# Kernel tuning notes

Measured on AMD Instinct MI355X. Metric: run time of the kernel, lower is better.

## Reference

```python
import jax, jax.numpy as jnp
import numpy as np

N_NODES = 50000
N_EDGES = 400000
N_GRAPHS = 500
N_FEAT = 4
EMB = 200
HID = 128


def setup_inputs() -> dict:
    key = jax.random.key(0)
    ks = jax.random.split(key, 16)
    x = jax.random.normal(ks[0], (N_NODES, N_FEAT), dtype=jnp.float32)
    edge_index = jax.random.randint(ks[1], (2, N_EDGES), 0, N_NODES, dtype=jnp.int64)
    x_scalar = jax.random.normal(ks[2], (N_GRAPHS, N_FEAT), dtype=jnp.float32)
    batch_index = jnp.sort(jax.random.randint(ks[3], (N_NODES,), 0, N_GRAPHS, dtype=jnp.int64))

    def lin(k, fan_in, fan_out):
        return jax.random.normal(k, (fan_in, fan_out), dtype=jnp.float32) / np.sqrt(fan_in)

    params = {
        'W0': lin(ks[4], N_FEAT, EMB), 'b0': jnp.zeros((EMB,), jnp.float32),
        'W1': lin(ks[5], EMB, EMB), 'b1': jnp.zeros((EMB,), jnp.float32),
        'W2': lin(ks[6], EMB, EMB), 'b2': jnp.zeros((EMB,), jnp.float32),
        'W3': lin(ks[7], EMB, EMB), 'b3': jnp.zeros((EMB,), jnp.float32),
        'Wl1': lin(ks[8], EMB + N_FEAT, HID),
        'bl1': jax.random.normal(ks[9], (HID,), jnp.float32) * 0.01,
        'Wl2': lin(ks[10], HID, 1),
        'bl2': jax.random.normal(ks[11], (1,), jnp.float32) * 0.01,
    }
    return dict(x=x, edge_index=edge_index, x_scalar=x_scalar, batch_index=batch_index, **params)


def _gcn_conv(h, W, b, src, dst, norm, num_nodes):
    # PyG GCNConv: h' = D^-1/2 (A+I) D^-1/2 (h W) + b, with precomputed edge norms
    m = (h @ W)[src] * norm[:, None]            # [E+N, out]
    out = jax.ops.segment_sum(m, dst, num_segments=num_nodes)
    return out + b


def reference(x, edge_index, x_scalar, batch_index,
              W0, b0, W1, b1, W2, b2, W3, b3, Wl1, bl1, Wl2, bl2):
    num_nodes = x.shape[0]
    loops = jnp.arange(num_nodes, dtype=edge_index.dtype)
    src = jnp.concatenate([edge_index[0], loops])  # self-loops appended
    dst = jnp.concatenate([edge_index[1], loops])
    deg = jax.ops.segment_sum(jnp.ones_like(dst, dtype=x.dtype), dst, num_segments=num_nodes)
    dinv = deg ** -0.5                              # deg >= 1 due to self-loops
    norm = dinv[src] * dinv[dst]

    h = jax.nn.leaky_relu(_gcn_conv(x, W0, b0, src, dst, norm, num_nodes), 0.01)
    h = jax.nn.leaky_relu(_gcn_conv(h, W1, b1, src, dst, norm, num_nodes), 0.01)
    h = jax.nn.leaky_relu(_gcn_conv(h, W2, b2, src, dst, norm, num_nodes), 0.01)
    h = jax.nn.leaky_relu(_gcn_conv(h, W3, b3, src, dst, norm, num_nodes), 0.01)

    # global mean pool per graph
    sums = jax.ops.segment_sum(h, batch_index, num_segments=N_GRAPHS)
    cnt = jax.ops.segment_sum(jnp.ones((num_nodes,), h.dtype), batch_index, num_segments=N_GRAPHS)
    pooled = sums / jnp.maximum(cnt, 1.0)[:, None]

    g = jnp.concatenate([pooled, x_scalar], axis=1)   # [G, EMB+4]
    g = jax.nn.leaky_relu(g @ Wl1 + bl1, 0.01)
    out = g @ Wl2 + bl2                                # [G, 1]
    return out
```

## Files before the change

### kernel.cpp

```cpp
#include <hip/hip_runtime.h>
#include <math.h>

#define LEAKY(v) ((v) > 0.0f ? (v) : 0.01f * (v))

typedef _Float16 v8h __attribute__((ext_vector_type(8)));
typedef float v4f __attribute__((ext_vector_type(4)));

__global__ void k_count(const int* __restrict__ ei, int* __restrict__ cnt, int E) {
    int e = blockIdx.x * blockDim.x + threadIdx.x;
    if (e < E) atomicAdd(&cnt[ei[E + e]], 1);
}

__global__ __launch_bounds__(256) void k_scan1(const int* __restrict__ cnt,
                                               int* __restrict__ rowptr,
                                               int* __restrict__ bsum, int n) {
    __shared__ int s[256];
    int t = threadIdx.x, i = blockIdx.x * 256 + t;
    int v = (i < n) ? cnt[i] : 0;
    s[t] = v;
    __syncthreads();
    for (int off = 1; off < 256; off <<= 1) {
        int u = (t >= off) ? s[t - off] : 0;
        __syncthreads();
        s[t] += u;
        __syncthreads();
    }
    if (i < n) rowptr[i] = s[t] - v;
    if (t == 255) bsum[blockIdx.x] = s[255];
}

__global__ __launch_bounds__(256) void k_scan3(int* __restrict__ rowptr,
                                               const int* __restrict__ bsum,
                                               const int* __restrict__ cnt,
                                               float* __restrict__ dinv, int n,
                                               float* __restrict__ pooled, int npool) {
    __shared__ int sred[256];
    int t = threadIdx.x;
    int accum = 0;
    for (int b = t; b < (int)blockIdx.x; b += 256) accum += bsum[b];
    sred[t] = accum;
    __syncthreads();
    for (int off = 128; off > 0; off >>= 1) {
        if (t < off) sred[t] += sred[t + off];
        __syncthreads();
    }
    int base = sred[0];
    int i = blockIdx.x * 256 + t;
    if (i < n) {
        rowptr[i] += base;
        dinv[i] = rsqrtf(1.0f + (float)cnt[i]);
    }
    for (int j = i; j < npool; j += gridDim.x * 256) pooled[j] = 0.0f;
}

__global__ void k_fill(const int* __restrict__ ei, const float* __restrict__ dinv,
                       int* __restrict__ rowptr, int2* __restrict__ adj, int E) {
    int e = blockIdx.x * blockDim.x + threadIdx.x;
    if (e < E) {
        int s = ei[e], d = ei[E + e];
        int pos = atomicAdd(&rowptr[d], 1);
        adj[pos] = make_int2(s, __float_as_int(dinv[s] * dinv[d]));
    }
}

__global__ __launch_bounds__(256) void k_splitW3(const float* __restrict__ W1,
                                                 const float* __restrict__ W2,
                                                 const float* __restrict__ W3,
                                                 _Float16* __restrict__ th0, _Float16* __restrict__ tl0,
                                                 _Float16* __restrict__ th1, _Float16* __restrict__ tl1,
                                                 _Float16* __restrict__ th2, _Float16* __restrict__ tl2,
                                                 int* __restrict__ cnt, int n) {
    int layer = blockIdx.y;
    const float* W = (layer == 0) ? W1 : (layer == 1) ? W2 : W3;
    _Float16* Wth = (layer == 0) ? th0 : (layer == 1) ? th1 : th2;
    _Float16* Wtl = (layer == 0) ? tl0 : (layer == 1) ? tl1 : tl2;
    int idx = blockIdx.x * blockDim.x + threadIdx.x;
    int gidx = (blockIdx.y * gridDim.x + blockIdx.x) * 256 + threadIdx.x;
    for (int j = gidx; j < n; j += gridDim.x * gridDim.y * 256) cnt[j] = 0;
    if (idx >= 224 * 208) return;
    int k = idx / 208, c = idx - k * 208;
    float v = (k < 200 && c < 200) ? W[k * 200 + c] : 0.0f;
    _Float16 hi = (_Float16)v;
    _Float16 lo = (_Float16)(v - (float)hi);
    Wth[c * 224 + k] = hi;
    Wtl[c * 224 + k] = lo;
}

__global__ __launch_bounds__(512, 4) void k_gemm200_mfma_l0(const float* __restrict__ x,
                                                            const float* __restrict__ dinv,
                                                            const int* __restrict__ rowptr,
                                                            const int2* __restrict__ adj,
                                                            const float* __restrict__ W0,
                                                            const float* __restrict__ b0,
                                                            const _Float16* __restrict__ Wth,
                                                            const _Float16* __restrict__ Wtl,
                                                            _Float16* __restrict__ T, int M) {
    __shared__ _Float16 Wsh[2][208 * 32];
    __shared__ _Float16 Wsl[2][208 * 32];
    __shared__ float W0s[4][200];
    __shared__ float b0s[200];
    const int tid  = threadIdx.x;
    const int lane = tid & 63;
    const int wid  = tid >> 6;
    const int quad = lane >> 4;
    const int l16  = lane & 15;
    const int rowA = blockIdx.x * 128 + wid * 16 + l16;
    const int rowAc = min(rowA, M - 1);

    const int nr0 = tid >> 2, p0 = tid & 3;
    const bool two = (tid < 320);
    const int nr1 = nr0 + 128;
    uint4 rh0, rl0, rh1, rl1;
    rh0 = *(const uint4*)&Wth[nr0 * 224 + p0 * 8];
    rl0 = *(const uint4*)&Wtl[nr0 * 224 + p0 * 8];
    if (two) {
        rh1 = *(const uint4*)&Wth[nr1 * 224 + p0 * 8];
        rl1 = *(const uint4*)&Wtl[nr1 * 224 + p0 * 8];
    }

    for (int idx = tid; idx < 1000; idx += 512) {
        if (idx < 800) W0s[idx / 200][idx % 200] = W0[idx];
        else b0s[idx - 800] = b0[idx - 800];
    }

    float w0n = dinv[rowAc]; w0n *= w0n;
    float4 xv = ((const float4*)x)[rowAc];
    float4 pxv = make_float4(xv.x * w0n, xv.y * w0n, xv.z * w0n, xv.w * w0n);
    {
        int lo = rowAc ? rowptr[rowAc - 1] : 0;
        int hi = rowptr[rowAc];
        for (int j = lo; j < hi; ++j) {
            int2 cw = adj[j];
            float w = __int_as_float(cw.y);
            float4 sv = ((const float4*)x)[cw.x];
            pxv.x += sv.x * w; pxv.y += sv.y * w; pxv.z += sv.z * w; pxv.w += sv.w * w;
        }
    }

    v4f acc[13];
#pragma unroll
    for (int t = 0; t < 13; ++t) acc[t] = 0.0f;

#pragma unroll
    for (int kc = 0; kc < 7; ++kc) {
        const int k0 = kc * 32;
        const int buf = kc & 1;
        *(uint4*)&Wsh[buf][nr0 * 32 + p0 * 8] = rh0;
        *(uint4*)&Wsl[buf][nr0 * 32 + p0 * 8] = rl0;
        if (two) {
            *(uint4*)&Wsh[buf][nr1 * 32 + p0 * 8] = rh1;
            *(uint4*)&Wsl[buf][nr1 * 32 + p0 * 8] = rl1;
        }
        if (kc < 6) {
            rh0 = *(const uint4*)&Wth[nr0 * 224 + (k0 + 32) + p0 * 8];
            rl0 = *(const uint4*)&Wtl[nr0 * 224 + (k0 + 32) + p0 * 8];
            if (two) {
                rh1 = *(const uint4*)&Wth[nr1 * 224 + (k0 + 32) + p0 * 8];
                rl1 = *(const uint4*)&Wtl[nr1 * 224 + (k0 + 32) + p0 * 8];
            }
        }
        __syncthreads();
        v8h ah, al;
        int kb = k0 + quad * 8;
        if (kb < 200) {
#pragma unroll
            for (int j = 0; j < 8; ++j) {
                int k = kb + j;
                float pv = pxv.x * W0s[0][k] + pxv.y * W0s[1][k]
                         + pxv.z * W0s[2][k] + pxv.w * W0s[3][k] + b0s[k];
                pv = LEAKY(pv);
                _Float16 h = (_Float16)pv;
                ah[j] = h;
                al[j] = (_Float16)(pv - (float)h);
            }
        } else {
#pragma unroll
            for (int j = 0; j < 8; ++j) { ah[j] = (_Float16)0.0f; al[j] = (_Float16)0.0f; }
        }
#pragma unroll
        for (int t = 0; t < 13; ++t) {
            int nidx = (t * 16 + l16) * 32 + quad * 8;
            v8h wh = *(const v8h*)&Wsh[buf][nidx];
            v8h wl = *(const v8h*)&Wsl[buf][nidx];
            acc[t] = __builtin_amdgcn_mfma_f32_16x16x32_f16(ah, wh, acc[t], 0, 0, 0);
            acc[t] = __builtin_amdgcn_mfma_f32_16x16x32_f16(ah, wl, acc[t], 0, 0, 0);
            acc[t] = __builtin_amdgcn_mfma_f32_16x16x32_f16(al, wh, acc[t], 0, 0, 0);
        }
    }
    const int rb = blockIdx.x * 128 + wid * 16 + quad * 4;
#pragma unroll
    for (int t = 0; t < 13; ++t) {
        int c = t * 16 + l16;
        if (c < 200) {
#pragma unroll
            for (int e = 0; e < 4; ++e) {
                int r = rb + e;
                if (r < M) T[(size_t)r * 200 + c] = (_Float16)acc[t][e];
            }
        }
    }
}

__global__ __launch_bounds__(512, 4) void k_gemm200_mfma(const _Float16* __restrict__ P,
                                                         const float* __restrict__ bias,
                                                         const _Float16* __restrict__ Wth,
                                                         const _Float16* __restrict__ Wtl,
                                                         _Float16* __restrict__ T, int M) {
    __shared__ _Float16 Wsh[2][208 * 32];
    __shared__ _Float16 Wsl[2][208 * 32];
    __shared__ float bS[200];
    const int tid  = threadIdx.x;
    const int lane = tid & 63;
    const int wid  = tid >> 6;
    const int quad = lane >> 4;
    const int l16  = lane & 15;
    const int rowA = blockIdx.x * 128 + wid * 16 + l16;
    const int rowAc = min(rowA, M - 1);
    const _Float16* Prow = P + (size_t)rowAc * 200;

    const int nr0 = tid >> 2, p0 = tid & 3;
    const bool two = (tid < 320);
    const int nr1 = nr0 + 128;
    uint4 rh0, rl0, rh1, rl1;
    rh0 = *(const uint4*)&Wth[nr0 * 224 + p0 * 8];
    rl0 = *(const uint4*)&Wtl[nr0 * 224 + p0 * 8];
    if (two) {
        rh1 = *(const uint4*)&Wth[nr1 * 224 + p0 * 8];
        rl1 = *(const uint4*)&Wtl[nr1 * 224 + p0 * 8];
    }
    if (tid < 200) bS[tid] = bias[tid];

    v8h pch[7];
#pragma unroll
    for (int kc = 0; kc < 7; ++kc) {
        int kb = kc * 32 + quad * 8;
        if (kb < 200) {
            pch[kc] = *(const v8h*)(Prow + kb);
        } else {
#pragma unroll
            for (int j = 0; j < 8; ++j) pch[kc][j] = (_Float16)0.0f;
        }
    }

    v4f acc[13];
#pragma unroll
    for (int t = 0; t < 13; ++t) acc[t] = 0.0f;

#pragma unroll
    for (int kc = 0; kc < 7; ++kc) {
        const int k0 = kc * 32;
        const int buf = kc & 1;
        *(uint4*)&Wsh[buf][nr0 * 32 + p0 * 8] = rh0;
        *(uint4*)&Wsl[buf][nr0 * 32 + p0 * 8] = rl0;
        if (two) {
            *(uint4*)&Wsh[buf][nr1 * 32 + p0 * 8] = rh1;
            *(uint4*)&Wsl[buf][nr1 * 32 + p0 * 8] = rl1;
        }
        if (kc < 6) {
            rh0 = *(const uint4*)&Wth[nr0 * 224 + (k0 + 32) + p0 * 8];
            rl0 = *(const uint4*)&Wtl[nr0 * 224 + (k0 + 32) + p0 * 8];
            if (two) {
                rh1 = *(const uint4*)&Wth[nr1 * 224 + (k0 + 32) + p0 * 8];
                rl1 = *(const uint4*)&Wtl[nr1 * 224 + (k0 + 32) + p0 * 8];
            }
        }
        __syncthreads();
        v8h ah, al;
        int kb = k0 + quad * 8;
        if (kb < 200) {
            v8h ph = pch[kc];
#pragma unroll
            for (int j = 0; j < 8; ++j) {
                float av = (float)ph[j] + bS[kb + j];
                av = LEAKY(av);
                _Float16 h = (_Float16)av;
                ah[j] = h;
                al[j] = (_Float16)(av - (float)h);
            }
        } else {
#pragma unroll
            for (int j = 0; j < 8; ++j) { ah[j] = (_Float16)0.0f; al[j] = (_Float16)0.0f; }
        }
#pragma unroll
        for (int t = 0; t < 13; ++t) {
            int nidx = (t * 16 + l16) * 32 + quad * 8;
            v8h wh = *(const v8h*)&Wsh[buf][nidx];
            v8h wl = *(const v8h*)&Wsl[buf][nidx];
            acc[t] = __builtin_amdgcn_mfma_f32_16x16x32_f16(ah, wh, acc[t], 0, 0, 0);
            acc[t] = __builtin_amdgcn_mfma_f32_16x16x32_f16(ah, wl, acc[t], 0, 0, 0);
            acc[t] = __builtin_amdgcn_mfma_f32_16x16x32_f16(al, wh, acc[t], 0, 0, 0);
        }
    }
    const int rb = blockIdx.x * 128 + wid * 16 + quad * 4;
#pragma unroll
    for (int t = 0; t < 13; ++t) {
        int c = t * 16 + l16;
        if (c < 200) {
#pragma unroll
            for (int e = 0; e < 4; ++e) {
                int r = rb + e;
                if (r < M) T[(size_t)r * 200 + c] = (_Float16)acc[t][e];
            }
        }
    }
}

__global__ __launch_bounds__(256) void k_gather200h(const _Float16* __restrict__ t,
                                                    const float* __restrict__ dinv,
                                                    const int* __restrict__ rowptr,
                                                    const int2* __restrict__ adj,
                                                    _Float16* __restrict__ p, int n) {
    int gid = blockIdx.x * blockDim.x + threadIdx.x;
    if (gid >= n * 25) return;
    int v = gid / 25, c8 = gid - v * 25;
    const v8h* tp = (const v8h*)t;
    float w0 = dinv[v]; w0 *= w0;
    v8h tv = tp[v * 25 + c8];
    float a0[8], a1[8], a2[8], a3[8];
#pragma unroll
    for (int i = 0; i < 8; ++i) { a0[i] = (float)tv[i] * w0; a1[i] = 0.0f; a2[i] = 0.0f; a3[i] = 0.0f; }
    int lo = v ? rowptr[v - 1] : 0;
    int hi = rowptr[v];
    int j = lo;
    for (; j + 3 < hi; j += 4) {
        int2 e0 = adj[j], e1 = adj[j + 1], e2 = adj[j + 2], e3 = adj[j + 3];
        float wa = __int_as_float(e0.y), wb = __int_as_float(e1.y);
        float wc = __int_as_float(e2.y), wd = __int_as_float(e3.y);
        v8h s0 = tp[e0.x * 25 + c8];
        v8h s1 = tp[e1.x * 25 + c8];
        v8h s2 = tp[e2.x * 25 + c8];
        v8h s3 = tp[e3.x * 25 + c8];
#pragma unroll
        for (int i = 0; i < 8; ++i) {
            a0[i] += (float)s0[i] * wa;
            a1[i] += (float)s1[i] * wb;
            a2[i] += (float)s2[i] * wc;
            a3[i] += (float)s3[i] * wd;
        }
    }
    for (; j < hi; ++j) {
        int2 cw = adj[j];
        float w = __int_as_float(cw.y);
        v8h sv = tp[cw.x * 25 + c8];
#pragma unroll
        for (int i = 0; i < 8; ++i) a0[i] += (float)sv[i] * w;
    }
    v8h o;
#pragma unroll
    for (int i = 0; i < 8; ++i) o[i] = (_Float16)((a0[i] + a1[i]) + (a2[i] + a3[i]));
    ((v8h*)p)[v * 25 + c8] = o;
}

__global__ __launch_bounds__(256) void k_gpool(const _Float16* __restrict__ T,
                                               const float* __restrict__ dinv,
                                               const int* __restrict__ rowptr,
                                               const int2* __restrict__ adj,
                                               const float* __restrict__ b3,
                                               const int* __restrict__ batch, int n,
                                               float* __restrict__ pooled) {
    __shared__ float part[10][25][9];
    const int t = threadIdx.x;
    const int c8 = t % 25, li = t / 25;
    const int base = blockIdx.x * 32;
    const int end = min(base + 32, n);
    const v8h* tp = (const v8h*)T;
    float4 ba = *(const float4*)(b3 + c8 * 8);
    float4 bb = *(const float4*)(b3 + c8 * 8 + 4);
    float bv[8] = {ba.x, ba.y, ba.z, ba.w, bb.x, bb.y, bb.z, bb.w};

    int seg = base;
    while (seg < end) {
        int g = batch[seg];
        int lo2 = seg + 1, hi2 = end;
        while (lo2 < hi2) { int m = (lo2 + hi2) >> 1; if (batch[m] == g) lo2 = m + 1; else hi2 = m; }
        int segend = lo2;

        if (li < 10) {
            float acc[8];
#pragma unroll
            for (int i = 0; i < 8; ++i) acc[i] = 0.0f;
            for (int i = seg + li; i < segend; i += 10) {
                float w0 = dinv[i]; w0 *= w0;
                v8h tv = tp[(size_t)i * 25 + c8];
                float a0[8], a1[8];
#pragma unroll
                for (int q = 0; q < 8; ++q) { a0[q] = (float)tv[q] * w0; a1[q] = 0.0f; }
                int elo = i ? rowptr[i - 1] : 0;
                int ehi = rowptr[i];
                int j = elo;
                for (; j + 1 < ehi; j += 2) {
                    int2 e0 = adj[j], e1 = adj[j + 1];
                    float wa = __int_as_float(e0.y), wb = __int_as_float(e1.y);
                    v8h s0 = tp[(size_t)e0.x * 25 + c8];
                    v8h s1 = tp[(size_t)e1.x * 25 + c8];
#pragma unroll
                    for (int q = 0; q < 8; ++q) {
                        a0[q] += (float)s0[q] * wa;
                        a1[q] += (float)s1[q] * wb;
                    }
                }
                if (j < ehi) {
                    int2 cw = adj[j];
                    float w = __int_as_float(cw.y);
                    v8h sv = tp[(size_t)cw.x * 25 + c8];
#pragma unroll
                    for (int q = 0; q < 8; ++q) a0[q] += (float)sv[q] * w;
                }
#pragma unroll
                for (int q = 0; q < 8; ++q) {
                    float v = a0[q] + a1[q] + bv[q];
                    acc[q] += LEAKY(v);
                }
            }
#pragma unroll
            for (int q = 0; q < 8; ++q) part[li][c8][q] = acc[q];
        }
        __syncthreads();
        if (t < 200) {
            float s = 0.0f;
#pragma unroll
            for (int l2 = 0; l2 < 10; ++l2) s += part[l2][t >> 3][t & 7];
            atomicAdd(&pooled[g * 200 + t], s);
        }
        __syncthreads();
        seg = segend;
    }
}

__global__ __launch_bounds__(128) void k_headfin(const float* __restrict__ pooled,
                                                 const int* __restrict__ batch, int n_nodes,
                                                 const float* __restrict__ xs,
                                                 const float* __restrict__ Wl1,
                                                 const float* __restrict__ bl1,
                                                 const float* __restrict__ Wl2,
                                                 const float* __restrict__ bl2,
                                                 float* __restrict__ out) {
    __shared__ float grow[204];
    __shared__ float partial[2];
    __shared__ int sb[2];
    int g = blockIdx.x;
    int t = threadIdx.x;
    if (t == 0 || t == 64) {
        int target = g + (t ? 1 : 0);
        int lo = 0, hi = n_nodes;
        while (lo < hi) { int m = (lo + hi) >> 1; if (batch[m] < target) lo = m + 1; else hi = m; }
        sb[t ? 1 : 0] = lo;
    }
    __syncthreads();
    float inv = 1.0f / fmaxf((float)(sb[1] - sb[0]), 1.0f);
    for (int idx = t; idx < 200; idx += 128) grow[idx] = pooled[g * 200 + idx] * inv;
    if (t < 4) grow[200 + t] = xs[g * 4 + t];
    __syncthreads();
    float s = bl1[t];
    for (int k = 0; k < 204; ++k) s += grow[k] * Wl1[k * 128 + t];
    s = LEAKY(s);
    float hv = s * Wl2[t];
    for (int off = 32; off > 0; off >>= 1) hv += __shfl_down(hv, off, 64);
    if ((t & 63) == 0) partial[t >> 6] = hv;
    __syncthreads();
    if (t == 0) out[g] = partial[0] + partial[1] + bl2[0];
}

extern "C" void kernel_launch(void* const* d_in, const int* in_sizes, int n_in,
                              void* d_out, int out_size, void* d_ws, size_t ws_size,
                              hipStream_t stream) {
    const float* x    = (const float*)d_in[0];
    const int*   ei   = (const int*)d_in[1];
    const float* xs   = (const float*)d_in[2];
    const int*   batch= (const int*)d_in[3];
    const float* W0   = (const float*)d_in[4];
    const float* b0   = (const float*)d_in[5];
    const float* W1   = (const float*)d_in[6];
    const float* b1   = (const float*)d_in[7];
    const float* W2   = (const float*)d_in[8];
    const float* b2   = (const float*)d_in[9];
    const float* W3   = (const float*)d_in[10];
    const float* b3   = (const float*)d_in[11];
    const float* Wl1  = (const float*)d_in[12];
    const float* bl1  = (const float*)d_in[13];
    const float* Wl2  = (const float*)d_in[14];
    const float* bl2  = (const float*)d_in[15];
    float* out = (float*)d_out;

    const int N = in_sizes[0] / 4;
    const int E = in_sizes[1] / 2;
    const int G = in_sizes[2] / 4;

    char* ws = (char*)d_ws;
    size_t off = 0;
    auto alloc = [&](size_t bytes) { void* p = ws + off; off += (bytes + 255) & ~size_t(255); return p; };
    _Float16* bufA = (_Float16*)alloc((size_t)N * 200 * sizeof(_Float16));
    _Float16* bufB = (_Float16*)alloc((size_t)N * 200 * sizeof(_Float16));
    float* dinv   = (float*)alloc((size_t)N * sizeof(float));
    float* pooled = (float*)alloc((size_t)G * 200 * sizeof(float));
    int*   cnt    = (int*)alloc((size_t)N * sizeof(int));
    int*   rowptr = (int*)alloc(((size_t)N + 1) * sizeof(int));
    int*   bsum   = (int*)alloc(256 * sizeof(int));
    int2*  adj    = (int2*)alloc((size_t)E * sizeof(int2));
    _Float16* Wth[3]; _Float16* Wtl[3];
    for (int i = 0; i < 3; ++i) {
        Wth[i] = (_Float16*)alloc(208 * 224 * sizeof(_Float16));
        Wtl[i] = (_Float16*)alloc(208 * 224 * sizeof(_Float16));
    }

    const int B = 256;
    const int nblk = (N + 255) / 256;

    dim3 sg((224 * 208 + B - 1) / B, 3);
    k_splitW3<<<sg, B, 0, stream>>>(W1, W2, W3, Wth[0], Wtl[0], Wth[1], Wtl[1], Wth[2], Wtl[2],
                                    cnt, N);

    k_count<<<(E + B - 1) / B, B, 0, stream>>>(ei, cnt, E);
    k_scan1<<<nblk, 256, 0, stream>>>(cnt, rowptr, bsum, N);
    k_scan3<<<nblk, 256, 0, stream>>>(rowptr, bsum, cnt, dinv, N, pooled, G * 200);
    k_fill<<<(E + B - 1) / B, B, 0, stream>>>(ei, dinv, rowptr, adj, E);

    const int gblocks = (N * 25 + 255) / 256;
    const int mblocks = (N + 127) / 128;

    k_gemm200_mfma_l0<<<mblocks, 512, 0, stream>>>(x, dinv, rowptr, adj, W0, b0,
                                                   Wth[0], Wtl[0], bufA, N);
    k_gather200h<<<gblocks, 256, 0, stream>>>(bufA, dinv, rowptr, adj, bufB, N);

    k_gemm200_mfma<<<mblocks, 512, 0, stream>>>(bufB, b1, Wth[1], Wtl[1], bufA, N);
    k_gather200h<<<gblocks, 256, 0, stream>>>(bufA, dinv, rowptr, adj, bufB, N);
    k_gemm200_mfma<<<mblocks, 512, 0, stream>>>(bufB, b2, Wth[2], Wtl[2], bufA, N);

    k_gpool<<<(N + 31) / 32, 256, 0, stream>>>(bufA, dinv, rowptr, adj, b3, batch, N, pooled);
    k_headfin<<<G, 128, 0, stream>>>(pooled, batch, N, xs, Wl1, bl1, Wl2, bl2, out);
}
```

Baseline: 328.3 us.

## Fuse degree count into weight split, single-pass scan, unroll pooling gather by four

Moves zeroing of the count and pooled buffers to memsets and folds the edge degree counting into the weight-split kernel, removing one launch. The two-kernel block scan becomes one kernel in which every block re-reduces all preceding counts from global memory, which saves a launch but adds redundant reads that grow with the block index. In the pooling gather, the neighbor loop is unrolled to four independent accumulators to expose more memory-level parallelism, at some register cost.

New measurement: 359.9 us. 9.6% more time.

```diff
diff --git a/kernel.cpp b/kernel.cpp
--- a/kernel.cpp
+++ b/kernel.cpp
@@ -6,16 +6,48 @@
 typedef _Float16 v8h __attribute__((ext_vector_type(8)));
 typedef float v4f __attribute__((ext_vector_type(4)));
 
-__global__ void k_count(const int* __restrict__ ei, int* __restrict__ cnt, int E) {
-    int e = blockIdx.x * blockDim.x + threadIdx.x;
-    if (e < E) atomicAdd(&cnt[ei[E + e]], 1);
-}
-
-__global__ __launch_bounds__(256) void k_scan1(const int* __restrict__ cnt,
-                                               int* __restrict__ rowptr,
-                                               int* __restrict__ bsum, int n) {
+__global__ __launch_bounds__(256) void k_splitcount(const float* __restrict__ W1,
+                                                    const float* __restrict__ W2,
+                                                    const float* __restrict__ W3,
+                                                    _Float16* __restrict__ th0, _Float16* __restrict__ tl0,
+                                                    _Float16* __restrict__ th1, _Float16* __restrict__ tl1,
+                                                    _Float16* __restrict__ th2, _Float16* __restrict__ tl2,
+                                                    const int* __restrict__ ei, int* __restrict__ cnt,
+                                                    int E) {
+    int layer = blockIdx.y;
+    const float* W = (layer == 0) ? W1 : (layer == 1) ? W2 : W3;
+    _Float16* Wth = (layer == 0) ? th0 : (layer == 1) ? th1 : th2;
+    _Float16* Wtl = (layer == 0) ? tl0 : (layer == 1) ? tl1 : tl2;
+    int idx = blockIdx.x * blockDim.x + threadIdx.x;
+    int gidx = (blockIdx.y * gridDim.x + blockIdx.x) * 256 + threadIdx.x;
+    int gsz = gridDim.x * gridDim.y * 256;
+    for (int e = gidx; e < E; e += gsz) atomicAdd(&cnt[ei[E + e]], 1);
+    if (idx >= 224 * 208) return;
+    int k = idx / 208, c = idx - k * 208;
+    float v = (k < 200 && c < 200) ? W[k * 200 + c] : 0.0f;
+    _Float16 hi = (_Float16)v;
+    _Float16 lo = (_Float16)(v - (float)hi);
+    Wth[c * 224 + k] = hi;
+    Wtl[c * 224 + k] = lo;
+}
+
+__global__ __launch_bounds__(256) void k_scan(const int* __restrict__ cnt,
+                                              int* __restrict__ rowptr,
+                                              float* __restrict__ dinv, int n) {
     __shared__ int s[256];
-    int t = threadIdx.x, i = blockIdx.x * 256 + t;
+    __shared__ int sred[256];
+    int t = threadIdx.x;
+    int lim = blockIdx.x * 256;
+    int accum = 0;
+    for (int i = t; i < lim; i += 256) accum += cnt[i];
+    sred[t] = accum;
+    __syncthreads();
+    for (int off = 128; off > 0; off >>= 1) {
+        if (t < off) sred[t] += sred[t + off];
+        __syncthreads();
+    }
+    int base = sred[0];
+    int i = lim + t;
     int v = (i < n) ? cnt[i] : 0;
     s[t] = v;
     __syncthreads();
@@ -25,32 +57,10 @@
         s[t] += u;
         __syncthreads();
     }
-    if (i < n) rowptr[i] = s[t] - v;
-    if (t == 255) bsum[blockIdx.x] = s[255];
-}
-
-__global__ __launch_bounds__(256) void k_scan3(int* __restrict__ rowptr,
-                                               const int* __restrict__ bsum,
-                                               const int* __restrict__ cnt,
-                                               float* __restrict__ dinv, int n,
-                                               float* __restrict__ pooled, int npool) {
-    __shared__ int sred[256];
-    int t = threadIdx.x;
-    int accum = 0;
-    for (int b = t; b < (int)blockIdx.x; b += 256) accum += bsum[b];
-    sred[t] = accum;
-    __syncthreads();
-    for (int off = 128; off > 0; off >>= 1) {
-        if (t < off) sred[t] += sred[t + off];
-        __syncthreads();
-    }
-    int base = sred[0];
-    int i = blockIdx.x * 256 + t;
     if (i < n) {
-        rowptr[i] += base;
-        dinv[i] = rsqrtf(1.0f + (float)cnt[i]);
-    }
-    for (int j = i; j < npool; j += gridDim.x * 256) pooled[j] = 0.0f;
+        rowptr[i] = base + s[t] - v;
+        dinv[i] = rsqrtf(1.0f + (float)v);
+    }
 }
 
 __global__ void k_fill(const int* __restrict__ ei, const float* __restrict__ dinv,
@@ -61,29 +71,6 @@
         int pos = atomicAdd(&rowptr[d], 1);
         adj[pos] = make_int2(s, __float_as_int(dinv[s] * dinv[d]));
     }
-}
-
-__global__ __launch_bounds__(256) void k_splitW3(const float* __restrict__ W1,
-                                                 const float* __restrict__ W2,
-                                                 const float* __restrict__ W3,
-                                                 _Float16* __restrict__ th0, _Float16* __restrict__ tl0,
-                                                 _Float16* __restrict__ th1, _Float16* __restrict__ tl1,
-                                                 _Float16* __restrict__ th2, _Float16* __restrict__ tl2,
-                                                 int* __restrict__ cnt, int n) {
-    int layer = blockIdx.y;
-    const float* W = (layer == 0) ? W1 : (layer == 1) ? W2 : W3;
-    _Float16* Wth = (layer == 0) ? th0 : (layer == 1) ? th1 : th2;
-    _Float16* Wtl = (layer == 0) ? tl0 : (layer == 1) ? tl1 : tl2;
-    int idx = blockIdx.x * blockDim.x + threadIdx.x;
-    int gidx = (blockIdx.y * gridDim.x + blockIdx.x) * 256 + threadIdx.x;
-    for (int j = gidx; j < n; j += gridDim.x * gridDim.y * 256) cnt[j] = 0;
-    if (idx >= 224 * 208) return;
-    int k = idx / 208, c = idx - k * 208;
-    float v = (k < 200 && c < 200) ? W[k * 200 + c] : 0.0f;
-    _Float16 hi = (_Float16)v;
-    _Float16 lo = (_Float16)(v - (float)hi);
-    Wth[c * 224 + k] = hi;
-    Wtl[c * 224 + k] = lo;
 }
 
 __global__ __launch_bounds__(512, 4) void k_gemm200_mfma_l0(const float* __restrict__ x,
@@ -382,24 +369,31 @@
             for (int i = seg + li; i < segend; i += 10) {
                 float w0 = dinv[i]; w0 *= w0;
                 v8h tv = tp[(size_t)i * 25 + c8];
-                float a0[8], a1[8];
-#pragma unroll
-                for (int q = 0; q < 8; ++q) { a0[q] = (float)tv[q] * w0; a1[q] = 0.0f; }
+                float a0[8], a1[8], a2[8], a3[8];
+#pragma unroll
+                for (int q = 0; q < 8; ++q) {
+                    a0[q] = (float)tv[q] * w0; a1[q] = 0.0f; a2[q] = 0.0f; a3[q] = 0.0f;
+                }
                 int elo = i ? rowptr[i - 1] : 0;
                 int ehi = rowptr[i];
                 int j = elo;
-                for (; j + 1 < ehi; j += 2) {
-                    int2 e0 = adj[j], e1 = adj[j + 1];
+                for (; j + 3 < ehi; j += 4) {
+                    int2 e0 = adj[j], e1 = adj[j + 1], e2 = adj[j + 2], e3 = adj[j + 3];
                     float wa = __int_as_float(e0.y), wb = __int_as_float(e1.y);
+                    float wc = __int_as_float(e2.y), wd = __int_as_float(e3.y);
                     v8h s0 = tp[(size_t)e0.x * 25 + c8];
                     v8h s1 = tp[(size_t)e1.x * 25 + c8];
+                    v8h s2 = tp[(size_t)e2.x * 25 + c8];
+                    v8h s3 = tp[(size_t)e3.x * 25 + c8];
 #pragma unroll
                     for (int q = 0; q < 8; ++q) {
                         a0[q] += (float)s0[q] * wa;
                         a1[q] += (float)s1[q] * wb;
+                        a2[q] += (float)s2[q] * wc;
+                        a3[q] += (float)s3[q] * wd;
                     }
                 }
-                if (j < ehi) {
+                for (; j < ehi; ++j) {
                     int2 cw = adj[j];
                     float w = __int_as_float(cw.y);
                     v8h sv = tp[(size_t)cw.x * 25 + c8];
@@ -408,7 +402,7 @@
                 }
 #pragma unroll
                 for (int q = 0; q < 8; ++q) {
-                    float v = a0[q] + a1[q] + bv[q];
+                    float v = (a0[q] + a1[q]) + (a2[q] + a3[q]) + bv[q];
                     acc[q] += LEAKY(v);
                 }
             }
@@ -495,7 +489,6 @@
     float* pooled = (float*)alloc((size_t)G * 200 * sizeof(float));
     int*   cnt    = (int*)alloc((size_t)N * sizeof(int));
     int*   rowptr = (int*)alloc(((size_t)N + 1) * sizeof(int));
-    int*   bsum   = (int*)alloc(256 * sizeof(int));
     int2*  adj    = (int2*)alloc((size_t)E * sizeof(int2));
     _Float16* Wth[3]; _Float16* Wtl[3];
     for (int i = 0; i < 3; ++i) {
@@ -506,13 +499,14 @@
     const int B = 256;
     const int nblk = (N + 255) / 256;
 
+    hipMemsetAsync(cnt, 0, (size_t)N * sizeof(int), stream);
+    hipMemsetAsync(pooled, 0, (size_t)G * 200 * sizeof(float), stream);
+
     dim3 sg((224 * 208 + B - 1) / B, 3);
-    k_splitW3<<<sg, B, 0, stream>>>(W1, W2, W3, Wth[0], Wtl[0], Wth[1], Wtl[1], Wth[2], Wtl[2],
-                                    cnt, N);
-
-    k_count<<<(E + B - 1) / B, B, 0, stream>>>(ei, cnt, E);
-    k_scan1<<<nblk, 256, 0, stream>>>(cnt, rowptr, bsum, N);
-    k_scan3<<<nblk, 256, 0, stream>>>(rowptr, bsum, cnt, dinv, N, pooled, G * 200);
+    k_splitcount<<<sg, B, 0, stream>>>(W1, W2, W3, Wth[0], Wtl[0], Wth[1], Wtl[1], Wth[2], Wtl[2],
+                                       ei, cnt, E);
+
+    k_scan<<<nblk, 256, 0, stream>>>(cnt, rowptr, dinv, N);
     k_fill<<<(E + B - 1) / B, B, 0, stream>>>(ei, dinv, rowptr, adj, E);
 
     const int gblocks = (N * 25 + 255) / 256;
```
